# Performance work log

Measured on AMD Instinct MI355X. Metric: run time of the kernel, lower is better.

Reference implementation:

```python
import jax, jax.numpy as jnp
import numpy as np

WIDTH = 128
N_NODE = 1024
N_REL = 12
OPS = ["Copy", "And", "Or", "Chaining", "Not"]


def setup_inputs() -> dict:
    key = jax.random.key(0)
    k1, k2, k3, k4, k5, k6 = jax.random.split(key, 6)
    return {
        "inputs": jax.random.uniform(k1, (WIDTH, N_NODE), dtype=jnp.float32),
        "database": jax.random.uniform(k2, (N_REL, N_NODE, N_NODE), dtype=jnp.float32),
        "arg1_weights": jax.random.normal(k3, (WIDTH, WIDTH), dtype=jnp.float32),
        "arg2_weights": jax.random.normal(k4, (WIDTH, WIDTH), dtype=jnp.float32),
        "op_weights": jax.random.normal(k5, (WIDTH, len(OPS)), dtype=jnp.float32),
        "chain_weights": jax.random.normal(k6, (WIDTH, 2 * N_REL), dtype=jnp.float32),
    }


def _chain(x, database, chain_weights):
    # x: [width, n_node], database: [n_rel, n, n], chain_weights: [width, 2*n_rel]
    n_rel = database.shape[0]
    cw = jax.nn.softmax(chain_weights, axis=1)
    w_fwd, w_bwd = cw[:, :n_rel], cw[:, n_rel:]  # [width, n_rel] each
    # Per-width relation-averaged adjacency: A[w,a,b] = sum_r D[r,a,b]*w_fwd[w,r] + D[r,b,a]*w_bwd[w,r]
    avg_rel = (jnp.einsum('rab,wr->wab', database, w_fwd)
               + jnp.einsum('rba,wr->wab', database, w_bwd))
    chained = jnp.einsum('wa,wab->wb', x, avg_rel)  # [width, n_node]
    return 1.0 - jnp.exp(-chained)


def reference(inputs, database, arg1_weights, arg2_weights, op_weights, chain_weights):
    # inputs: [width, n_node] fuzzy truth values
    arg1 = jax.nn.softmax(arg1_weights, axis=0).T @ inputs  # [width, n_node]
    arg2 = jax.nn.softmax(arg2_weights, axis=0).T @ inputs
    opw = jax.nn.softmax(op_weights, axis=1).T  # [n_ops, width]

    out = jnp.zeros_like(inputs)
    for i, op in enumerate(OPS):
        if op == 'Copy':
            res = arg2
        elif op == 'And':
            res = arg1 * arg2
        elif op == 'Or':
            res = arg1 + arg2 - arg1 * arg2
        elif op == 'Chaining':
            res = _chain(arg2, database, chain_weights)
        elif op == 'Not':
            res = 1.0 - arg1
        out = out + res * opw[i][:, None]
    return out
```

## Files before the change

kernel.cpp:

```cpp
#include <hip/hip_runtime.h>
#include <math.h>

#define W128  128
#define NNODE 1024
#define NREL  12
#define TS    72

#define OFF_S1T   0
#define OFF_S2T   16384
#define OFF_OPW   32768
#define OFF_WF    33408
#define OFF_WB    34944
#define OFF_ARG1  36480
#define OFF_ARG2  167552
#define OFF_ARG2B 298624
#define OFF_PART  364160

typedef short bf16x8 __attribute__((ext_vector_type(8)));
typedef short short4v __attribute__((ext_vector_type(4)));
typedef float f32x4  __attribute__((ext_vector_type(4)));

__device__ __forceinline__ short bf16t(float x) {
    return (short)(__float_as_uint(x) >> 16);
}
__device__ __forceinline__ float bf16f(short s) {
    return __uint_as_float((unsigned)(unsigned short)s << 16);
}
__device__ __forceinline__ unsigned pk2(float lo, float hi) {
    return (__float_as_uint(hi) & 0xFFFF0000u) | (__float_as_uint(lo) >> 16);
}

__global__ __launch_bounds__(128) void k_prep(const float* __restrict__ a1w,
                                              const float* __restrict__ a2w,
                                              const float* __restrict__ opww,
                                              const float* __restrict__ chw,
                                              float* __restrict__ ws) {
    __shared__ float wred[2];
    int b = blockIdx.x;
    int j = threadIdx.x;
    if (b < 256) {
        int col = b & 127;
        const float* src = (b < 128) ? a1w : a2w;
        float* dst = ws + ((b < 128) ? OFF_S1T : OFF_S2T);
        float v = src[j * W128 + col];
        float m = v;
#pragma unroll
        for (int off = 32; off; off >>= 1) m = fmaxf(m, __shfl_xor(m, off));
        if ((j & 63) == 0) wred[j >> 6] = m;
        __syncthreads();
        m = fmaxf(wred[0], wred[1]);
        float e = expf(v - m);
        float s = e;
#pragma unroll
        for (int off = 32; off; off >>= 1) s += __shfl_xor(s, off);
        __syncthreads();
        if ((j & 63) == 0) wred[j >> 6] = s;
        __syncthreads();
        s = wred[0] + wred[1];
        dst[col * W128 + j] = e / s;
    } else {
        int i = j;
        float v[5], mx = -1e30f;
        for (int k = 0; k < 5; ++k) { v[k] = opww[i * 5 + k]; mx = fmaxf(mx, v[k]); }
        float s = 0.f;
        for (int k = 0; k < 5; ++k) { v[k] = expf(v[k] - mx); s += v[k]; }
        float inv = 1.0f / s;
        for (int k = 0; k < 5; ++k) ws[OFF_OPW + k * W128 + i] = v[k] * inv;
        float u[24]; mx = -1e30f;
        for (int k = 0; k < 24; ++k) { u[k] = chw[i * 24 + k]; mx = fmaxf(mx, u[k]); }
        s = 0.f;
        for (int k = 0; k < 24; ++k) { u[k] = expf(u[k] - mx); s += u[k]; }
        inv = 1.0f / s;
        for (int k = 0; k < 12; ++k) ws[OFF_WF + i * NREL + k] = u[k] * inv;
        for (int k = 0; k < 12; ++k) ws[OFF_WB + i * NREL + k] = u[12 + k] * inv;
    }
}

__global__ __launch_bounds__(256) void k_args2(const float* __restrict__ inputs,
                                               float* __restrict__ ws,
                                               short* __restrict__ x2b) {
    __shared__ float lin[128 * 33];
    int t = threadIdx.x;
    int n0 = blockIdx.x * 32;
    int w0 = blockIdx.y * 16;
#pragma unroll
    for (int u = 0; u < 16; ++u) {
        int idx = t + u * 256;
        int j = idx >> 5, nn = idx & 31;
        lin[j * 33 + nn] = inputs[j * NNODE + n0 + nn];
    }
    __syncthreads();
    int nn = t & 31;
    int n = n0 + nn;
    int wA = w0 + (t >> 5);
    int wB = wA + 8;
    const float* s1A = ws + OFF_S1T + wA * W128;
    const float* s2A = ws + OFF_S2T + wA * W128;
    const float* s1B = ws + OFF_S1T + wB * W128;
    const float* s2B = ws + OFF_S2T + wB * W128;
    float a1A = 0.f, a2A = 0.f, a1B = 0.f, a2B = 0.f;
#pragma unroll 4
    for (int j = 0; j < W128; ++j) {
        float in = lin[j * 33 + nn];
        a1A = fmaf(s1A[j], in, a1A);
        a2A = fmaf(s2A[j], in, a2A);
        a1B = fmaf(s1B[j], in, a1B);
        a2B = fmaf(s2B[j], in, a2B);
    }
    ws[OFF_ARG1 + wA * NNODE + n] = a1A;
    ws[OFF_ARG2 + wA * NNODE + n] = a2A;
    ws[OFF_ARG1 + wB * NNODE + n] = a1B;
    ws[OFF_ARG2 + wB * NNODE + n] = a2B;
    x2b[wA * NNODE + n] = bf16t(a2A);
    x2b[wB * NNODE + n] = bf16t(a2B);
}

__global__ __launch_bounds__(512) void k_chain3(const float* __restrict__ db,
                                                const float* __restrict__ ws,
                                                const short* __restrict__ x2b,
                                                short* __restrict__ partF,
                                                short* __restrict__ partB) {
    __shared__ __align__(16) short Tf[64 * TS];
    __shared__ __align__(16) short Tt[64 * TS];
    const float* wf = ws + OFF_WF;
    const float* wb = ws + OFF_WB;

    int tid = threadIdx.x;
    int l   = tid & 63, wid = tid >> 6;
    int wm  = wid >> 2;
    int wn  = wid & 3;
    int l16 = l & 15, lq = l >> 4;
    int B0  = blockIdx.x * 64;
    int A0  = blockIdx.y * 64;

    bf16x8 bfF[2][2], bfB[2][2];
#pragma unroll
    for (int ni = 0; ni < 2; ++ni)
#pragma unroll
        for (int ks = 0; ks < 2; ++ks) {
            int w = wn * 32 + ni * 16 + l16;
            bfF[ni][ks] = *(const bf16x8*)&x2b[w * NNODE + A0 + ks * 32 + lq * 8];
            bfB[ni][ks] = *(const bf16x8*)&x2b[w * NNODE + B0 + ks * 32 + lq * 8];
        }

    f32x4 accF[2][2], accB[2][2];
#pragma unroll
    for (int mi = 0; mi < 2; ++mi)
#pragma unroll
        for (int ni = 0; ni < 2; ++ni) {
            accF[mi][ni] = (f32x4){0.f, 0.f, 0.f, 0.f};
            accB[mi][ni] = (f32x4){0.f, 0.f, 0.f, 0.f};
        }

    int a0 = 2 * (tid >> 4);
    int c0 = 4 * (tid & 15);
    const float* gbase = db + (size_t)(A0 + a0) * NNODE + B0 + c0;
    const size_t rstep = (size_t)NNODE * NNODE;

    float4 g0 = *(const float4*)(gbase);
    float4 g1 = *(const float4*)(gbase + NNODE);

#pragma unroll 2
    for (int r = 0; r < NREL; ++r) {
        uint2 p0 = {pk2(g0.x, g0.y), pk2(g0.z, g0.w)};
        uint2 p1 = {pk2(g1.x, g1.y), pk2(g1.z, g1.w)};
        *(uint2*)&Tf[a0 * TS + c0]       = p0;
        *(uint2*)&Tf[(a0 + 1) * TS + c0] = p1;
        *(unsigned*)&Tt[(c0 + 0) * TS + a0] = pk2(g0.x, g1.x);
        *(unsigned*)&Tt[(c0 + 1) * TS + a0] = pk2(g0.y, g1.y);
        *(unsigned*)&Tt[(c0 + 2) * TS + a0] = pk2(g0.z, g1.z);
        *(unsigned*)&Tt[(c0 + 3) * TS + a0] = pk2(g0.w, g1.w);
        __syncthreads();

        float4 n0v = g0, n1v = g1;
        if (r + 1 < NREL) {
            const float* g = gbase + (size_t)(r + 1) * rstep;
            n0v = *(const float4*)(g);
            n1v = *(const float4*)(g + NNODE);
        }

        f32x4 tF[2][2], tB[2][2];
#pragma unroll
        for (int mi = 0; mi < 2; ++mi)
#pragma unroll
            for (int ni = 0; ni < 2; ++ni) {
                tF[mi][ni] = (f32x4){0.f, 0.f, 0.f, 0.f};
                tB[mi][ni] = (f32x4){0.f, 0.f, 0.f, 0.f};
            }

#pragma unroll
        for (int ks = 0; ks < 2; ++ks) {
            bf16x8 AF[2], AB[2];
#pragma unroll
            for (int mi = 0; mi < 2; ++mi) {
                int row = wm * 32 + mi * 16 + l16;
                int off = ks * 32 + lq * 8;
                AF[mi] = *(const bf16x8*)&Tt[row * TS + off];
                AB[mi] = *(const bf16x8*)&Tf[row * TS + off];
            }
#pragma unroll
            for (int mi = 0; mi < 2; ++mi)
#pragma unroll
                for (int ni = 0; ni < 2; ++ni) {
                    tF[mi][ni] = __builtin_amdgcn_mfma_f32_16x16x32_bf16(
                        AF[mi], bfF[ni][ks], tF[mi][ni], 0, 0, 0);
                    tB[mi][ni] = __builtin_amdgcn_mfma_f32_16x16x32_bf16(
                        AB[mi], bfB[ni][ks], tB[mi][ni], 0, 0, 0);
                }
        }
        __syncthreads();

#pragma unroll
        for (int ni = 0; ni < 2; ++ni) {
            int w = wn * 32 + ni * 16 + l16;
            float wfv = wf[w * NREL + r];
            float wbv = wb[w * NREL + r];
#pragma unroll
            for (int mi = 0; mi < 2; ++mi)
#pragma unroll
                for (int v = 0; v < 4; ++v) {
                    accF[mi][ni][v] += wfv * tF[mi][ni][v];
                    accB[mi][ni][v] += wbv * tB[mi][ni][v];
                }
        }
        g0 = n0v; g1 = n1v;
    }

#pragma unroll
    for (int mi = 0; mi < 2; ++mi)
#pragma unroll
        for (int v = 0; v < 4; ++v) {
            int m = wm * 32 + mi * 16 + lq * 4 + v;
#pragma unroll
            for (int ni = 0; ni < 2; ++ni) {
                int w = wn * 32 + ni * 16 + l16;
                partF[(size_t)blockIdx.y * (NNODE * W128) + (B0 + m) * W128 + w]
                    = bf16t(accF[mi][ni][v]);
                partB[(size_t)blockIdx.x * (NNODE * W128) + (A0 + m) * W128 + w]
                    = bf16t(accB[mi][ni][v]);
            }
        }
}

__global__ __launch_bounds__(256) void k_reduce3(const float* __restrict__ ws,
                                                 const short* __restrict__ partF,
                                                 const short* __restrict__ partB,
                                                 float* __restrict__ out) {
    __shared__ float chs[64 * 17];
    int t = threadIdx.x;
    int n0 = blockIdx.x * 64;
    int w0 = blockIdx.y * 16;
    {
        int n_loc = t >> 2;
        int wq = (t & 3) * 4;
        size_t base = (size_t)(n0 + n_loc) * W128 + w0 + wq;
        float c0 = 0.f, c1 = 0.f, c2 = 0.f, c3 = 0.f;
#pragma unroll
        for (int s = 0; s < 16; ++s) {
            short4v pf = *(const short4v*)&partF[(size_t)s * (NNODE * W128) + base];
            short4v pb = *(const short4v*)&partB[(size_t)s * (NNODE * W128) + base];
            c0 += bf16f(pf[0]) + bf16f(pb[0]);
            c1 += bf16f(pf[1]) + bf16f(pb[1]);
            c2 += bf16f(pf[2]) + bf16f(pb[2]);
            c3 += bf16f(pf[3]) + bf16f(pb[3]);
        }
        chs[n_loc * 17 + wq + 0] = c0;
        chs[n_loc * 17 + wq + 1] = c1;
        chs[n_loc * 17 + wq + 2] = c2;
        chs[n_loc * 17 + wq + 3] = c3;
    }
    __syncthreads();
    {
        int w_loc = t >> 4;
        int n4 = (t & 15) * 4;
        int w = w0 + w_loc;
        float ch[4];
#pragma unroll
        for (int j = 0; j < 4; ++j) ch[j] = chs[(n4 + j) * 17 + w_loc];
        float4 a1 = *(const float4*)&ws[OFF_ARG1 + w * NNODE + n0 + n4];
        float4 a2 = *(const float4*)&ws[OFF_ARG2 + w * NNODE + n0 + n4];
        float o0 = ws[OFF_OPW + 0 * W128 + w];
        float o1 = ws[OFF_OPW + 1 * W128 + w];
        float o2 = ws[OFF_OPW + 2 * W128 + w];
        float o3 = ws[OFF_OPW + 3 * W128 + w];
        float o4 = ws[OFF_OPW + 4 * W128 + w];
        float a1v[4] = {a1.x, a1.y, a1.z, a1.w};
        float a2v[4] = {a2.x, a2.y, a2.z, a2.w};
        float ov[4];
#pragma unroll
        for (int j = 0; j < 4; ++j) {
            float p = a1v[j] * a2v[j];
            ov[j] = o0 * a2v[j] + o1 * p + o2 * (a1v[j] + a2v[j] - p)
                  + o3 * (1.0f - expf(-ch[j])) + o4 * (1.0f - a1v[j]);
        }
        float4 o = {ov[0], ov[1], ov[2], ov[3]};
        *(float4*)&out[w * NNODE + n0 + n4] = o;
    }
}

extern "C" void kernel_launch(void* const* d_in, const int* in_sizes, int n_in,
                              void* d_out, int out_size, void* d_ws, size_t ws_size,
                              hipStream_t stream) {
    const float* inputs = (const float*)d_in[0];
    const float* db     = (const float*)d_in[1];
    const float* a1w    = (const float*)d_in[2];
    const float* a2w    = (const float*)d_in[3];
    const float* opww   = (const float*)d_in[4];
    const float* chw    = (const float*)d_in[5];
    float* ws  = (float*)d_ws;
    float* out = (float*)d_out;
    short* x2b   = (short*)(ws + OFF_ARG2B);
    short* partF = (short*)(ws + OFF_PART);
    short* partB = partF + (size_t)16 * NNODE * W128;

    hipLaunchKernelGGL(k_prep, dim3(257), dim3(128), 0, stream, a1w, a2w, opww, chw, ws);
    hipLaunchKernelGGL(k_args2, dim3(32, 8), dim3(256), 0, stream, inputs, ws, x2b);
    hipLaunchKernelGGL(k_chain3, dim3(16, 16), dim3(512), 0, stream,
                       db, ws, x2b, partF, partB);
    hipLaunchKernelGGL(k_reduce3, dim3(16, 8), dim3(256), 0, stream,
                       ws, partF, partB, out);
}
```

Before: 41.23 us.

## Fuse all four stages into one cooperative kernel with grid syncs

Replaces the four separate launches (prep, args, chain, reduce) with a single cooperative kernel of 256 blocks that uses grid.sync between phases. The softmaxes are recomputed locally inside each phase, so the separate prep pass and its workspace round trip go away, and the first database tile is prefetched before the first grid sync to overlap with the barrier. This targets launch overhead and inter-kernel gaps, at the cost of grid-wide barrier latency, redundant softmax work in every block, and a less vectorised reduce phase.

After: 111.4 us. 170% more time.

```diff
diff --git a/kernel.cpp b/kernel.cpp
--- a/kernel.cpp
+++ b/kernel.cpp
@@ -1,23 +1,20 @@
 #include <hip/hip_runtime.h>
+#include <hip/hip_cooperative_groups.h>
 #include <math.h>
+
+namespace cg = cooperative_groups;
 
 #define W128  128
 #define NNODE 1024
 #define NREL  12
 #define TS    72
 
-#define OFF_S1T   0
-#define OFF_S2T   16384
-#define OFF_OPW   32768
-#define OFF_WF    33408
-#define OFF_WB    34944
-#define OFF_ARG1  36480
-#define OFF_ARG2  167552
-#define OFF_ARG2B 298624
-#define OFF_PART  364160
+#define OFF_ARG1  0
+#define OFF_ARG2  131072
+#define OFF_ARG2B 262144
+#define OFF_PART  327680
 
 typedef short bf16x8 __attribute__((ext_vector_type(8)));
-typedef short short4v __attribute__((ext_vector_type(4)));
 typedef float f32x4  __attribute__((ext_vector_type(4)));
 
 __device__ __forceinline__ short bf16t(float x) {
@@ -30,271 +27,226 @@
     return (__float_as_uint(hi) & 0xFFFF0000u) | (__float_as_uint(lo) >> 16);
 }
 
-__global__ __launch_bounds__(128) void k_prep(const float* __restrict__ a1w,
-                                              const float* __restrict__ a2w,
-                                              const float* __restrict__ opww,
-                                              const float* __restrict__ chw,
-                                              float* __restrict__ ws) {
-    __shared__ float wred[2];
-    int b = blockIdx.x;
-    int j = threadIdx.x;
-    if (b < 256) {
-        int col = b & 127;
-        const float* src = (b < 128) ? a1w : a2w;
-        float* dst = ws + ((b < 128) ? OFF_S1T : OFF_S2T);
-        float v = src[j * W128 + col];
-        float m = v;
-#pragma unroll
-        for (int off = 32; off; off >>= 1) m = fmaxf(m, __shfl_xor(m, off));
-        if ((j & 63) == 0) wred[j >> 6] = m;
+__global__ __launch_bounds__(512) void k_fused(
+        const float* __restrict__ inputs, const float* __restrict__ db,
+        const float* __restrict__ a1w,    const float* __restrict__ a2w,
+        const float* __restrict__ opww,   const float* __restrict__ chw,
+        float* __restrict__ ws, short* __restrict__ x2b,
+        short* __restrict__ partF, short* __restrict__ partB,
+        float* __restrict__ out) {
+    __shared__ __align__(16) char smem[33536];
+    cg::grid_group grid = cg::this_grid();
+    int t   = threadIdx.x;
+    int bid = blockIdx.x;
+
+    {
+        float* lin = (float*)smem;
+        float* sm1 = (float*)(smem + 16896);
+        float* sm2 = sm1 + 16 * W128;
+        int n0 = (bid & 31) * 32;
+        int w0 = (bid >> 5) * 16;
+#pragma unroll
+        for (int u = 0; u < 8; ++u) {
+            int idx = t + u * 512;
+            int j = idx >> 5, nn = idx & 31;
+            lin[j * 33 + nn] = inputs[j * NNODE + n0 + nn];
+        }
+        {
+            int c = t >> 4, i = t & 15;
+            const float* src = (c < 16) ? a1w : a2w;
+            float* dst = (c < 16) ? sm1 : sm2;
+            int w_loc = c & 15;
+            int wcol = w0 + w_loc;
+            float v[8]; float mx = -1e30f;
+#pragma unroll
+            for (int k = 0; k < 8; ++k) {
+                v[k] = src[(i * 8 + k) * W128 + wcol];
+                mx = fmaxf(mx, v[k]);
+            }
+#pragma unroll
+            for (int off = 8; off; off >>= 1) mx = fmaxf(mx, __shfl_xor(mx, off));
+            float s = 0.f;
+#pragma unroll
+            for (int k = 0; k < 8; ++k) { v[k] = expf(v[k] - mx); s += v[k]; }
+#pragma unroll
+            for (int off = 8; off; off >>= 1) s += __shfl_xor(s, off);
+            float inv = 1.0f / s;
+#pragma unroll
+            for (int k = 0; k < 8; ++k) dst[w_loc * W128 + i * 8 + k] = v[k] * inv;
+        }
         __syncthreads();
-        m = fmaxf(wred[0], wred[1]);
-        float e = expf(v - m);
-        float s = e;
-#pragma unroll
-        for (int off = 32; off; off >>= 1) s += __shfl_xor(s, off);
-        __syncthreads();
-        if ((j & 63) == 0) wred[j >> 6] = s;
-        __syncthreads();
-        s = wred[0] + wred[1];
-        dst[col * W128 + j] = e / s;
-    } else {
-        int i = j;
-        float v[5], mx = -1e30f;
-        for (int k = 0; k < 5; ++k) { v[k] = opww[i * 5 + k]; mx = fmaxf(mx, v[k]); }
-        float s = 0.f;
-        for (int k = 0; k < 5; ++k) { v[k] = expf(v[k] - mx); s += v[k]; }
-        float inv = 1.0f / s;
-        for (int k = 0; k < 5; ++k) ws[OFF_OPW + k * W128 + i] = v[k] * inv;
-        float u[24]; mx = -1e30f;
-        for (int k = 0; k < 24; ++k) { u[k] = chw[i * 24 + k]; mx = fmaxf(mx, u[k]); }
-        s = 0.f;
-        for (int k = 0; k < 24; ++k) { u[k] = expf(u[k] - mx); s += u[k]; }
-        inv = 1.0f / s;
-        for (int k = 0; k < 12; ++k) ws[OFF_WF + i * NREL + k] = u[k] * inv;
-        for (int k = 0; k < 12; ++k) ws[OFF_WB + i * NREL + k] = u[12 + k] * inv;
+        int nn = t & 31, w_loc = t >> 5;
+        int n = n0 + nn, w = w0 + w_loc;
+        const float* s1 = sm1 + w_loc * W128;
+        const float* s2 = sm2 + w_loc * W128;
+        float a1 = 0.f, a2 = 0.f;
+#pragma unroll 4
+        for (int j = 0; j < W128; ++j) {
+            float in = lin[j * 33 + nn];
+            a1 = fmaf(s1[j], in, a1);
+            a2 = fmaf(s2[j], in, a2);
+        }
+        ws[OFF_ARG1 + w * NNODE + n] = a1;
+        ws[OFF_ARG2 + w * NNODE + n] = a2;
+        x2b[w * NNODE + n] = bf16t(a2);
     }
-}
-
-__global__ __launch_bounds__(256) void k_args2(const float* __restrict__ inputs,
-                                               float* __restrict__ ws,
-                                               short* __restrict__ x2b) {
-    __shared__ float lin[128 * 33];
-    int t = threadIdx.x;
-    int n0 = blockIdx.x * 32;
-    int w0 = blockIdx.y * 16;
-#pragma unroll
-    for (int u = 0; u < 16; ++u) {
-        int idx = t + u * 256;
-        int j = idx >> 5, nn = idx & 31;
-        lin[j * 33 + nn] = inputs[j * NNODE + n0 + nn];
-    }
-    __syncthreads();
-    int nn = t & 31;
-    int n = n0 + nn;
-    int wA = w0 + (t >> 5);
-    int wB = wA + 8;
-    const float* s1A = ws + OFF_S1T + wA * W128;
-    const float* s2A = ws + OFF_S2T + wA * W128;
-    const float* s1B = ws + OFF_S1T + wB * W128;
-    const float* s2B = ws + OFF_S2T + wB * W128;
-    float a1A = 0.f, a2A = 0.f, a1B = 0.f, a2B = 0.f;
-#pragma unroll 4
-    for (int j = 0; j < W128; ++j) {
-        float in = lin[j * 33 + nn];
-        a1A = fmaf(s1A[j], in, a1A);
-        a2A = fmaf(s2A[j], in, a2A);
-        a1B = fmaf(s1B[j], in, a1B);
-        a2B = fmaf(s2B[j], in, a2B);
-    }
-    ws[OFF_ARG1 + wA * NNODE + n] = a1A;
-    ws[OFF_ARG2 + wA * NNODE + n] = a2A;
-    ws[OFF_ARG1 + wB * NNODE + n] = a1B;
-    ws[OFF_ARG2 + wB * NNODE + n] = a2B;
-    x2b[wA * NNODE + n] = bf16t(a2A);
-    x2b[wB * NNODE + n] = bf16t(a2B);
-}
-
-__global__ __launch_bounds__(512) void k_chain3(const float* __restrict__ db,
-                                                const float* __restrict__ ws,
-                                                const short* __restrict__ x2b,
-                                                short* __restrict__ partF,
-                                                short* __restrict__ partB) {
-    __shared__ __align__(16) short Tf[64 * TS];
-    __shared__ __align__(16) short Tt[64 * TS];
-    const float* wf = ws + OFF_WF;
-    const float* wb = ws + OFF_WB;
-
-    int tid = threadIdx.x;
-    int l   = tid & 63, wid = tid >> 6;
-    int wm  = wid >> 2;
-    int wn  = wid & 3;
-    int l16 = l & 15, lq = l >> 4;
-    int B0  = blockIdx.x * 64;
-    int A0  = blockIdx.y * 64;
-
-    bf16x8 bfF[2][2], bfB[2][2];
-#pragma unroll
-    for (int ni = 0; ni < 2; ++ni)
-#pragma unroll
-        for (int ks = 0; ks < 2; ++ks) {
-            int w = wn * 32 + ni * 16 + l16;
-            bfF[ni][ks] = *(const bf16x8*)&x2b[w * NNODE + A0 + ks * 32 + lq * 8];
-            bfB[ni][ks] = *(const bf16x8*)&x2b[w * NNODE + B0 + ks * 32 + lq * 8];
-        }
-
-    f32x4 accF[2][2], accB[2][2];
-#pragma unroll
-    for (int mi = 0; mi < 2; ++mi)
-#pragma unroll
-        for (int ni = 0; ni < 2; ++ni) {
-            accF[mi][ni] = (f32x4){0.f, 0.f, 0.f, 0.f};
-            accB[mi][ni] = (f32x4){0.f, 0.f, 0.f, 0.f};
-        }
-
-    int a0 = 2 * (tid >> 4);
-    int c0 = 4 * (tid & 15);
+
+    int bx = bid & 15, by = bid >> 4;
+    int B0 = bx * 64, A0 = by * 64;
+    int a0 = 2 * (t >> 4), c0 = 4 * (t & 15);
     const float* gbase = db + (size_t)(A0 + a0) * NNODE + B0 + c0;
     const size_t rstep = (size_t)NNODE * NNODE;
-
     float4 g0 = *(const float4*)(gbase);
     float4 g1 = *(const float4*)(gbase + NNODE);
 
+    grid.sync();
+
+    {
+        short* Tf  = (short*)smem;
+        short* Tt  = Tf + 64 * TS;
+        float* wfs = (float*)(smem + 18432);
+        float* wbs = wfs + 128 * NREL;
+
+        if (t < 128) {
+            float u[24]; float mx = -1e30f;
+            for (int k = 0; k < 24; ++k) { u[k] = chw[t * 24 + k]; mx = fmaxf(mx, u[k]); }
+            float s = 0.f;
+            for (int k = 0; k < 24; ++k) { u[k] = expf(u[k] - mx); s += u[k]; }
+            float inv = 1.0f / s;
+            for (int k = 0; k < 12; ++k) wfs[t * NREL + k] = u[k] * inv;
+            for (int k = 0; k < 12; ++k) wbs[t * NREL + k] = u[12 + k] * inv;
+        }
+
+        int l   = t & 63, wid = t >> 6;
+        int wm  = wid >> 2;
+        int wn  = wid & 3;
+        int l16 = l & 15, lq = l >> 4;
+
+        bf16x8 bfF[2][2], bfB[2][2];
+#pragma unroll
+        for (int ni = 0; ni < 2; ++ni)
+#pragma unroll
+            for (int ks = 0; ks < 2; ++ks) {
+                int w = wn * 32 + ni * 16 + l16;
+                bfF[ni][ks] = *(const bf16x8*)&x2b[w * NNODE + A0 + ks * 32 + lq * 8];
+                bfB[ni][ks] = *(const bf16x8*)&x2b[w * NNODE + B0 + ks * 32 + lq * 8];
+            }
+
+        f32x4 accF[2][2], accB[2][2];
+#pragma unroll
+        for (int mi = 0; mi < 2; ++mi)
+#pragma unroll
+            for (int ni = 0; ni < 2; ++ni) {
+                accF[mi][ni] = (f32x4){0.f, 0.f, 0.f, 0.f};
+                accB[mi][ni] = (f32x4){0.f, 0.f, 0.f, 0.f};
+            }
+
 #pragma unroll 2
-    for (int r = 0; r < NREL; ++r) {
-        uint2 p0 = {pk2(g0.x, g0.y), pk2(g0.z, g0.w)};
-        uint2 p1 = {pk2(g1.x, g1.y), pk2(g1.z, g1.w)};
-        *(uint2*)&Tf[a0 * TS + c0]       = p0;
-        *(uint2*)&Tf[(a0 + 1) * TS + c0] = p1;
-        *(unsigned*)&Tt[(c0 + 0) * TS + a0] = pk2(g0.x, g1.x);
-        *(unsigned*)&Tt[(c0 + 1) * TS + a0] = pk2(g0.y, g1.y);
-        *(unsigned*)&Tt[(c0 + 2) * TS + a0] = pk2(g0.z, g1.z);
-        *(unsigned*)&Tt[(c0 + 3) * TS + a0] = pk2(g0.w, g1.w);
-        __syncthreads();
-
-        float4 n0v = g0, n1v = g1;
-        if (r + 1 < NREL) {
-            const float* g = gbase + (size_t)(r + 1) * rstep;
-            n0v = *(const float4*)(g);
-            n1v = *(const float4*)(g + NNODE);
-        }
-
-        f32x4 tF[2][2], tB[2][2];
-#pragma unroll
-        for (int mi = 0; mi < 2; ++mi)
-#pragma unroll
-            for (int ni = 0; ni < 2; ++ni) {
-                tF[mi][ni] = (f32x4){0.f, 0.f, 0.f, 0.f};
-                tB[mi][ni] = (f32x4){0.f, 0.f, 0.f, 0.f};
-            }
-
-#pragma unroll
-        for (int ks = 0; ks < 2; ++ks) {
-            bf16x8 AF[2], AB[2];
-#pragma unroll
-            for (int mi = 0; mi < 2; ++mi) {
-                int row = wm * 32 + mi * 16 + l16;
-                int off = ks * 32 + lq * 8;
-                AF[mi] = *(const bf16x8*)&Tt[row * TS + off];
-                AB[mi] = *(const bf16x8*)&Tf[row * TS + off];
-            }
+        for (int r = 0; r < NREL; ++r) {
+            uint2 p0 = {pk2(g0.x, g0.y), pk2(g0.z, g0.w)};
+            uint2 p1 = {pk2(g1.x, g1.y), pk2(g1.z, g1.w)};
+            *(uint2*)&Tf[a0 * TS + c0]       = p0;
+            *(uint2*)&Tf[(a0 + 1) * TS + c0] = p1;
+            *(unsigned*)&Tt[(c0 + 0) * TS + a0] = pk2(g0.x, g1.x);
+            *(unsigned*)&Tt[(c0 + 1) * TS + a0] = pk2(g0.y, g1.y);
+            *(unsigned*)&Tt[(c0 + 2) * TS + a0] = pk2(g0.z, g1.z);
+            *(unsigned*)&Tt[(c0 + 3) * TS + a0] = pk2(g0.w, g1.w);
+            __syncthreads();
+
+            float4 n0v = g0, n1v = g1;
+            if (r + 1 < NREL) {
+                const float* g = gbase + (size_t)(r + 1) * rstep;
+                n0v = *(const float4*)(g);
+                n1v = *(const float4*)(g + NNODE);
+            }
+
+            f32x4 tF[2][2], tB[2][2];
 #pragma unroll
             for (int mi = 0; mi < 2; ++mi)
 #pragma unroll
                 for (int ni = 0; ni < 2; ++ni) {
-                    tF[mi][ni] = __builtin_amdgcn_mfma_f32_16x16x32_bf16(
-                        AF[mi], bfF[ni][ks], tF[mi][ni], 0, 0, 0);
-                    tB[mi][ni] = __builtin_amdgcn_mfma_f32_16x16x32_bf16(
-                        AB[mi], bfB[ni][ks], tB[mi][ni], 0, 0, 0);
+                    tF[mi][ni] = (f32x4){0.f, 0.f, 0.f, 0.f};
+                    tB[mi][ni] = (f32x4){0.f, 0.f, 0.f, 0.f};
                 }
-        }
-        __syncthreads();
-
-#pragma unroll
-        for (int ni = 0; ni < 2; ++ni) {
-            int w = wn * 32 + ni * 16 + l16;
-            float wfv = wf[w * NREL + r];
-            float wbv = wb[w * NREL + r];
-#pragma unroll
-            for (int mi = 0; mi < 2; ++mi)
-#pragma unroll
-                for (int v = 0; v < 4; ++v) {
-                    accF[mi][ni][v] += wfv * tF[mi][ni][v];
-                    accB[mi][ni][v] += wbv * tB[mi][ni][v];
+
+#pragma unroll
+            for (int ks = 0; ks < 2; ++ks) {
+                bf16x8 AF[2], AB[2];
+#pragma unroll
+                for (int mi = 0; mi < 2; ++mi) {
+                    int row = wm * 32 + mi * 16 + l16;
+                    int off = ks * 32 + lq * 8;
+                    AF[mi] = *(const bf16x8*)&Tt[row * TS + off];
+                    AB[mi] = *(const bf16x8*)&Tf[row * TS + off];
                 }
-        }
-        g0 = n0v; g1 = n1v;
-    }
-
-#pragma unroll
-    for (int mi = 0; mi < 2; ++mi)
-#pragma unroll
-        for (int v = 0; v < 4; ++v) {
-            int m = wm * 32 + mi * 16 + lq * 4 + v;
+#pragma unroll
+                for (int mi = 0; mi < 2; ++mi)
+#pragma unroll
+                    for (int ni = 0; ni < 2; ++ni) {
+                        tF[mi][ni] = __builtin_amdgcn_mfma_f32_16x16x32_bf16(
+                            AF[mi], bfF[ni][ks], tF[mi][ni], 0, 0, 0);
+                        tB[mi][ni] = __builtin_amdgcn_mfma_f32_16x16x32_bf16(
+                            AB[mi], bfB[ni][ks], tB[mi][ni], 0, 0, 0);
+                    }
+            }
+            __syncthreads();
+
 #pragma unroll
             for (int ni = 0; ni < 2; ++ni) {
                 int w = wn * 32 + ni * 16 + l16;
-                partF[(size_t)blockIdx.y * (NNODE * W128) + (B0 + m) * W128 + w]
-                    = bf16t(accF[mi][ni][v]);
-                partB[(size_t)blockIdx.x * (NNODE * W128) + (A0 + m) * W128 + w]
-                    = bf16t(accB[mi][ni][v]);
-            }
-        }
-}
-
-__global__ __launch_bounds__(256) void k_reduce3(const float* __restrict__ ws,
-                                                 const short* __restrict__ partF,
-                                                 const short* __restrict__ partB,
-                                                 float* __restrict__ out) {
-    __shared__ float chs[64 * 17];
-    int t = threadIdx.x;
-    int n0 = blockIdx.x * 64;
-    int w0 = blockIdx.y * 16;
+                float wfv = wfs[w * NREL + r];
+                float wbv = wbs[w * NREL + r];
+#pragma unroll
+                for (int mi = 0; mi < 2; ++mi)
+#pragma unroll
+                    for (int v = 0; v < 4; ++v) {
+                        accF[mi][ni][v] += wfv * tF[mi][ni][v];
+                        accB[mi][ni][v] += wbv * tB[mi][ni][v];
+                    }
+            }
+            g0 = n0v; g1 = n1v;
+        }
+
+#pragma unroll
+        for (int mi = 0; mi < 2; ++mi)
+#pragma unroll
+            for (int v = 0; v < 4; ++v) {
+                int m = wm * 32 + mi * 16 + lq * 4 + v;
+#pragma unroll
+                for (int ni = 0; ni < 2; ++ni) {
+                    int w = wn * 32 + ni * 16 + l16;
+                    partF[(size_t)by * (NNODE * W128) + (B0 + m) * W128 + w]
+                        = bf16t(accF[mi][ni][v]);
+                    partB[(size_t)bx * (NNODE * W128) + (A0 + m) * W128 + w]
+                        = bf16t(accB[mi][ni][v]);
+                }
+            }
+    }
+
+    grid.sync();
+
     {
-        int n_loc = t >> 2;
-        int wq = (t & 3) * 4;
-        size_t base = (size_t)(n0 + n_loc) * W128 + w0 + wq;
-        float c0 = 0.f, c1 = 0.f, c2 = 0.f, c3 = 0.f;
+        int w = t & 127;
+        int n = (bid << 2) + (t >> 7);
+        size_t base = (size_t)n * W128 + w;
+        float ch = 0.f;
 #pragma unroll
         for (int s = 0; s < 16; ++s) {
-            short4v pf = *(const short4v*)&partF[(size_t)s * (NNODE * W128) + base];
-            short4v pb = *(const short4v*)&partB[(size_t)s * (NNODE * W128) + base];
-            c0 += bf16f(pf[0]) + bf16f(pb[0]);
-            c1 += bf16f(pf[1]) + bf16f(pb[1]);
-            c2 += bf16f(pf[2]) + bf16f(pb[2]);
-            c3 += bf16f(pf[3]) + bf16f(pb[3]);
-        }
-        chs[n_loc * 17 + wq + 0] = c0;
-        chs[n_loc * 17 + wq + 1] = c1;
-        chs[n_loc * 17 + wq + 2] = c2;
-        chs[n_loc * 17 + wq + 3] = c3;
-    }
-    __syncthreads();
-    {
-        int w_loc = t >> 4;
-        int n4 = (t & 15) * 4;
-        int w = w0 + w_loc;
-        float ch[4];
-#pragma unroll
-        for (int j = 0; j < 4; ++j) ch[j] = chs[(n4 + j) * 17 + w_loc];
-        float4 a1 = *(const float4*)&ws[OFF_ARG1 + w * NNODE + n0 + n4];
-        float4 a2 = *(const float4*)&ws[OFF_ARG2 + w * NNODE + n0 + n4];
-        float o0 = ws[OFF_OPW + 0 * W128 + w];
-        float o1 = ws[OFF_OPW + 1 * W128 + w];
-        float o2 = ws[OFF_OPW + 2 * W128 + w];
-        float o3 = ws[OFF_OPW + 3 * W128 + w];
-        float o4 = ws[OFF_OPW + 4 * W128 + w];
-        float a1v[4] = {a1.x, a1.y, a1.z, a1.w};
-        float a2v[4] = {a2.x, a2.y, a2.z, a2.w};
-        float ov[4];
-#pragma unroll
-        for (int j = 0; j < 4; ++j) {
-            float p = a1v[j] * a2v[j];
-            ov[j] = o0 * a2v[j] + o1 * p + o2 * (a1v[j] + a2v[j] - p)
-                  + o3 * (1.0f - expf(-ch[j])) + o4 * (1.0f - a1v[j]);
-        }
-        float4 o = {ov[0], ov[1], ov[2], ov[3]};
-        *(float4*)&out[w * NNODE + n0 + n4] = o;
+            ch += bf16f(partF[(size_t)s * (NNODE * W128) + base])
+                + bf16f(partB[(size_t)s * (NNODE * W128) + base]);
+        }
+        float v[5], mx = -1e30f;
+#pragma unroll
+        for (int k = 0; k < 5; ++k) { v[k] = opww[w * 5 + k]; mx = fmaxf(mx, v[k]); }
+        float s5 = 0.f;
+#pragma unroll
+        for (int k = 0; k < 5; ++k) { v[k] = expf(v[k] - mx); s5 += v[k]; }
+        float inv = 1.0f / s5;
+        float a1 = ws[OFF_ARG1 + w * NNODE + n];
+        float a2 = ws[OFF_ARG2 + w * NNODE + n];
+        float p = a1 * a2;
+        out[w * NNODE + n] = inv * (v[0] * a2 + v[1] * p + v[2] * (a1 + a2 - p)
+                           + v[3] * (1.0f - expf(-ch)) + v[4] * (1.0f - a1));
     }
 }
 
@@ -313,10 +265,9 @@
     short* partF = (short*)(ws + OFF_PART);
     short* partB = partF + (size_t)16 * NNODE * W128;
 
-    hipLaunchKernelGGL(k_prep, dim3(257), dim3(128), 0, stream, a1w, a2w, opww, chw, ws);
-    hipLaunchKernelGGL(k_args2, dim3(32, 8), dim3(256), 0, stream, inputs, ws, x2b);
-    hipLaunchKernelGGL(k_chain3, dim3(16, 16), dim3(512), 0, stream,
-                       db, ws, x2b, partF, partB);
-    hipLaunchKernelGGL(k_reduce3, dim3(16, 8), dim3(256), 0, stream,
-                       ws, partF, partB, out);
-}
+    void* kargs[] = {(void*)&inputs, (void*)&db, (void*)&a1w, (void*)&a2w,
+                     (void*)&opww, (void*)&chw, (void*)&ws, (void*)&x2b,
+                     (void*)&partF, (void*)&partB, (void*)&out};
+    hipLaunchCooperativeKernel((const void*)k_fused, dim3(256), dim3(512),
+                               kargs, 0, stream);
+}
```
